# Optimization experiments

Measured on AMD Instinct MI355X. Metric: run time of the kernel, lower is better.

The kernel has to match this reference:

```python
import jax, jax.numpy as jnp
import numpy as np

N = 100000      # nodes
E = 3200000     # edges (before self-loops)
IN = 1          # input feature dim
H1, C = 4, 8    # layer1: 4 heads x 8 channels; layer2: 1 head x 8 channels
NEG_SLOPE = 0.2


def setup_inputs() -> dict:
    key = jax.random.key(0)
    ks = jax.random.split(key, 10)
    x = jax.random.normal(ks[0], (N, IN), jnp.float32)
    edge_index = jax.random.randint(ks[1], (2, E), 0, N, dtype=jnp.int32)
    # layer 1 params (GATConv(1, 8, heads=4))
    W1 = jax.random.normal(ks[2], (IN, H1 * C), jnp.float32) * 0.5
    a_src1 = jax.random.normal(ks[3], (H1, C), jnp.float32) * 0.5
    a_dst1 = jax.random.normal(ks[4], (H1, C), jnp.float32) * 0.5
    b1 = jnp.zeros((H1 * C,), jnp.float32)
    # layer 2 params (GATConv(32, 8, heads=1))
    W2 = jax.random.normal(ks[5], (H1 * C, C), jnp.float32) * 0.2
    a_src2 = jax.random.normal(ks[6], (1, C), jnp.float32) * 0.5
    a_dst2 = jax.random.normal(ks[7], (1, C), jnp.float32) * 0.5
    b2 = jnp.zeros((C,), jnp.float32)
    return {"x": x, "edge_index": edge_index, "W1": W1, "a_src1": a_src1,
            "a_dst1": a_dst1, "b1": b1, "W2": W2, "a_src2": a_src2,
            "a_dst2": a_dst2, "b2": b2}


def _gat_layer(x, src, dst, W, a_s, a_d, b, heads, ch):
    # Linear transform per head: [N, heads, ch]
    h = (x @ W).reshape(-1, heads, ch)
    # per-node attention logits
    al_s = jnp.einsum('nhc,hc->nh', h, a_s)  # [N, H]
    al_d = jnp.einsum('nhc,hc->nh', h, a_d)  # [N, H]
    # per-edge logits (message src -> dst)
    e = jax.nn.leaky_relu(al_s[src] + al_d[dst], NEG_SLOPE)  # [E', H]
    # segment softmax over incoming edges of each dst node
    m = jax.ops.segment_max(e, dst, num_segments=N)          # [N, H]
    e = jnp.exp(e - m[dst])
    s = jax.ops.segment_sum(e, dst, num_segments=N)          # [N, H]
    alpha = e / s[dst]                                       # [E', H]
    # weighted scatter-add aggregation
    out = jax.ops.segment_sum(h[src] * alpha[:, :, None], dst, num_segments=N)
    return out.reshape(N, heads * ch) + b


def reference(x, edge_index, W1, a_src1, a_dst1, b1, W2, a_src2, a_dst2, b2):
    loops = jnp.arange(N, dtype=edge_index.dtype)
    src = jnp.concatenate([edge_index[0], loops])  # add self-loops (PyG default)
    dst = jnp.concatenate([edge_index[1], loops])
    h = _gat_layer(x, src, dst, W1, a_src1, a_dst1, b1, H1, C)
    h = jax.nn.relu(h)
    out = _gat_layer(h, src, dst, W2, a_src2, a_dst2, b2, 1, C)
    return out
```

## Files before the change

kernel.cpp:

```cpp
#include <hip/hip_runtime.h>
#include <hip/hip_bf16.h>

#define NEG_SLOPE 0.2f
#define CAP 6144
#define CAPG 8192


__global__ void init_cc(int* __restrict__ gcursor,
                        const float* __restrict__ W1,
                        const float* __restrict__ as1,
                        const float* __restrict__ ad1,
                        float* __restrict__ consts) {
    int t = threadIdx.x;
    if (t < 8) {
        int h = t & 3;
        const float* a = (t < 4) ? as1 : ad1;
        float s = 0.f;
        #pragma unroll
        for (int c = 0; c < 8; ++c)
            s += W1[h * 8 + c] * a[h * 8 + c];
        consts[t] = s;
    }
    gcursor[t] = t << 13;
}

__global__ void bucket_scatter(const int* __restrict__ ei, int* __restrict__ gcursor,
                               unsigned int* __restrict__ pairs, int E) {
    __shared__ int cnt[1024];
    __shared__ int basel[1024];
    int t = threadIdx.x;
    int chunk = (E + gridDim.x - 1) / gridDim.x;
    int lo = blockIdx.x * chunk;
    int hi = min(E, lo + chunk);
    const int* dei = ei + E;
    cnt[t] = 0;
    __syncthreads();
    bool vec = ((E & 3) == 0);
    int lo4 = (lo + 3) & ~3;
    int end4 = hi & ~3;
    if (vec && end4 > lo4) {
        for (int e = lo + t; e < lo4; e += 1024)
            atomicAdd(&cnt[dei[e] >> 7], 1);
        const int4* dei4 = (const int4*)dei;
        for (int v = (lo4 >> 2) + t; v < (end4 >> 2); v += 1024) {
            int4 d = dei4[v];
            atomicAdd(&cnt[d.x >> 7], 1);
            atomicAdd(&cnt[d.y >> 7], 1);
            atomicAdd(&cnt[d.z >> 7], 1);
            atomicAdd(&cnt[d.w >> 7], 1);
        }
        for (int e = end4 + t; e < hi; e += 1024)
            atomicAdd(&cnt[dei[e] >> 7], 1);
    } else {
        for (int e = lo + t; e < hi; e += 1024)
            atomicAdd(&cnt[dei[e] >> 7], 1);
    }
    __syncthreads();
    {
        int c = cnt[t];
        basel[t] = c ? (atomicAdd(&gcursor[t], c) - (t << 13)) : 0;
        cnt[t] = 0;
    }
    __syncthreads();
    if (vec && end4 > lo4) {
        for (int e = lo + t; e < lo4; e += 1024) {
            int s = ei[e], d = dei[e];
            int bk = d >> 7;
            int off = basel[bk] + atomicAdd(&cnt[bk], 1);
            if (off < CAPG) pairs[(bk << 13) + off] = (unsigned)s | ((unsigned)(d & 127) << 17);
        }
        const int4* sei4 = (const int4*)ei;
        const int4* dei4 = (const int4*)dei;
        for (int v = (lo4 >> 2) + t; v < (end4 >> 2); v += 1024) {
            int4 sv = sei4[v];
            int4 dv = dei4[v];
            int bk0 = dv.x >> 7, bk1 = dv.y >> 7, bk2 = dv.z >> 7, bk3 = dv.w >> 7;
            int o0 = basel[bk0] + atomicAdd(&cnt[bk0], 1);
            if (o0 < CAPG) pairs[(bk0 << 13) + o0] = (unsigned)sv.x | ((unsigned)(dv.x & 127) << 17);
            int o1 = basel[bk1] + atomicAdd(&cnt[bk1], 1);
            if (o1 < CAPG) pairs[(bk1 << 13) + o1] = (unsigned)sv.y | ((unsigned)(dv.y & 127) << 17);
            int o2 = basel[bk2] + atomicAdd(&cnt[bk2], 1);
            if (o2 < CAPG) pairs[(bk2 << 13) + o2] = (unsigned)sv.z | ((unsigned)(dv.z & 127) << 17);
            int o3 = basel[bk3] + atomicAdd(&cnt[bk3], 1);
            if (o3 < CAPG) pairs[(bk3 << 13) + o3] = (unsigned)sv.w | ((unsigned)(dv.w & 127) << 17);
        }
        for (int e = end4 + t; e < hi; e += 1024) {
            int s = ei[e], d = dei[e];
            int bk = d >> 7;
            int off = basel[bk] + atomicAdd(&cnt[bk], 1);
            if (off < CAPG) pairs[(bk << 13) + off] = (unsigned)s | ((unsigned)(d & 127) << 17);
        }
    } else {
        for (int e = lo + t; e < hi; e += 1024) {
            int s = ei[e], d = dei[e];
            int bk = d >> 7;
            int off = basel[bk] + atomicAdd(&cnt[bk], 1);
            if (off < CAPG) pairs[(bk << 13) + off] = (unsigned)s | ((unsigned)(d & 127) << 17);
        }
    }
}

__global__ void l1_comb(const float* __restrict__ x,
                        const int* __restrict__ gcursor,
                        const unsigned int* __restrict__ pairs,
                        const float* __restrict__ consts,
                        const float* __restrict__ W1, const float* __restrict__ b1,
                        const float* __restrict__ W2,
                        const float* __restrict__ as2, const float* __restrict__ ad2,
                        float* __restrict__ h2, float* __restrict__ als2,
                        float* __restrict__ ald2, int N) {
    __shared__ unsigned sbuf[CAP];
    __shared__ int hcnt[128], offs[128], hcur[128];
    __shared__ float xl[128];
    int t = threadIdx.x;
    int bk = blockIdx.x;
    int node0 = bk << 7;
    int nw = min(128, N - node0);
    if (t < 128) xl[t] = (t < nw) ? x[node0 + t] : 0.f;
    float S[4], D[4];
    #pragma unroll
    for (int h = 0; h < 4; ++h) { S[h] = consts[h]; D[h] = consts[4 + h]; }
    int base = bk << 13;
    int cnt_total = min(gcursor[bk] - base, CAPG);
    int g = t >> 2, j = t & 3;
    float sacc[4] = {0.f, 0.f, 0.f, 0.f};
    float tacc[4] = {0.f, 0.f, 0.f, 0.f};
    __syncthreads();
    float xd = xl[g];
    for (int c0 = 0; c0 < cnt_total; c0 += CAP) {
        int clen = min(CAP, cnt_total - c0);
        unsigned pr[12];
        #pragma unroll
        for (int k = 0; k < 12; ++k) {
            int idx = t + (k << 9);
            pr[k] = (idx < clen) ? pairs[base + c0 + idx] : 0xFFFFFFFFu;
        }
        if (t < 128) hcnt[t] = 0;
        __syncthreads();
        #pragma unroll
        for (int k = 0; k < 12; ++k)
            if (pr[k] != 0xFFFFFFFFu) atomicAdd(&hcnt[pr[k] >> 17], 1);
        __syncthreads();
        if (t < 64) {
            int h0 = hcnt[2 * t], h1 = hcnt[2 * t + 1];
            int s = h0 + h1, sc_ = s;
            #pragma unroll
            for (int o = 1; o < 64; o <<= 1) {
                int u = __shfl_up(sc_, o);
                if (t >= o) sc_ += u;
            }
            int excl = sc_ - s;
            offs[2 * t] = excl;          hcur[2 * t] = excl;
            offs[2 * t + 1] = excl + h0; hcur[2 * t + 1] = excl + h0;
        }
        __syncthreads();
        #pragma unroll
        for (int k = 0; k < 12; ++k)
            if (pr[k] != 0xFFFFFFFFu) {
                int loc = atomicAdd(&hcur[pr[k] >> 17], 1);
                sbuf[loc] = pr[k];
            }
        __syncthreads();
        int st = offs[g], en = st + hcnt[g];
        int i = st + j;
        float xs0 = 0.f, xs1 = 0.f;
        if (i < en) xs0 = x[sbuf[i] & 131071u];
        if (i + 4 < en) xs1 = x[sbuf[i + 4] & 131071u];
        for (; i < en; i += 4) {
            float xs = xs0;
            xs0 = xs1;
            int i2 = i + 8;
            xs1 = (i2 < en) ? x[sbuf[i2] & 131071u] : 0.f;
            #pragma unroll
            for (int h = 0; h < 4; ++h) {
                float v = xs * S[h] + xd * D[h];
                v = (v > 0.f) ? v : NEG_SLOPE * v;
                float w = __expf(v);
                sacc[h] += w;
                tacc[h] = fmaf(w, xs, tacc[h]);
            }
        }
        __syncthreads();
    }
    #pragma unroll
    for (int h = 0; h < 4; ++h) {
        sacc[h] += __shfl_xor(sacc[h], 1); sacc[h] += __shfl_xor(sacc[h], 2);
        tacc[h] += __shfl_xor(tacc[h], 1); tacc[h] += __shfl_xor(tacc[h], 2);
    }
    if (j == 0 && g < nw) {
        int n = node0 + g;
        float xn = xd;
        float o[8];
        #pragma unroll
        for (int c = 0; c < 8; ++c) o[c] = 0.f;
        #pragma unroll
        for (int h = 0; h < 4; ++h) {
            float v = xn * (S[h] + D[h]);
            v = (v > 0.f) ? v : NEG_SLOPE * v;
            float ww = __expf(v);
            float s1 = ww + sacc[h];
            float t1 = ww * xn + tacc[h];
            float tt = t1 / s1;
            #pragma unroll
            for (int c = 0; c < 8; ++c) {
                float rr = fmaxf(tt * W1[h * 8 + c] + b1[h * 8 + c], 0.f);
                #pragma unroll
                for (int c2 = 0; c2 < 8; ++c2) o[c2] += rr * W2[(h * 8 + c) * 8 + c2];
            }
        }
        float as = 0.f, ad = 0.f;
        #pragma unroll
        for (int c = 0; c < 8; ++c) { as += o[c] * as2[c]; ad += o[c] * ad2[c]; }
        float4* hv = (float4*)&h2[(size_t)n * 8];
        hv[0] = make_float4(o[0], o[1], o[2], o[3]);
        hv[1] = make_float4(o[4], o[5], o[6], o[7]);
        als2[n] = as;
        ald2[n] = ad;
    }
}

__global__ void l2_comb(const int* __restrict__ gcursor,
                        const unsigned int* __restrict__ pairs,
                        const float* __restrict__ als2, const float* __restrict__ ald2,
                        const float* __restrict__ h2, const float* __restrict__ b2,
                        float* __restrict__ out, int N) {
    __shared__ unsigned sbuf[CAP];
    __shared__ int hcnt[128], offs[128], hcur[128];
    __shared__ float adl[128];
    int t = threadIdx.x;
    int bk = blockIdx.x;
    int node0 = bk << 7;
    int nw = min(128, N - node0);
    if (t < 128) adl[t] = (t < nw) ? ald2[node0 + t] : 0.f;
    int base = bk << 13;
    int cnt_total = min(gcursor[bk] - base, CAPG);
    int g = t >> 2, j = t & 3;
    float acc[9];
    #pragma unroll
    for (int c = 0; c < 9; ++c) acc[c] = 0.f;
    __syncthreads();
    float adv = adl[g];
    for (int c0 = 0; c0 < cnt_total; c0 += CAP) {
        int clen = min(CAP, cnt_total - c0);
        unsigned pr[12];
        #pragma unroll
        for (int k = 0; k < 12; ++k) {
            int idx = t + (k << 9);
            pr[k] = (idx < clen) ? pairs[base + c0 + idx] : 0xFFFFFFFFu;
        }
        if (t < 128) hcnt[t] = 0;
        __syncthreads();
        #pragma unroll
        for (int k = 0; k < 12; ++k)
            if (pr[k] != 0xFFFFFFFFu) atomicAdd(&hcnt[pr[k] >> 17], 1);
        __syncthreads();
        if (t < 64) {
            int h0 = hcnt[2 * t], h1 = hcnt[2 * t + 1];
            int s = h0 + h1, sc_ = s;
            #pragma unroll
            for (int o = 1; o < 64; o <<= 1) {
                int u = __shfl_up(sc_, o);
                if (t >= o) sc_ += u;
            }
            int excl = sc_ - s;
            offs[2 * t] = excl;          hcur[2 * t] = excl;
            offs[2 * t + 1] = excl + h0; hcur[2 * t + 1] = excl + h0;
        }
        __syncthreads();
        #pragma unroll
        for (int k = 0; k < 12; ++k)
            if (pr[k] != 0xFFFFFFFFu) {
                int loc = atomicAdd(&hcur[pr[k] >> 17], 1);
                sbuf[loc] = pr[k];
            }
        __syncthreads();
        int st = offs[g], en = st + hcnt[g];
        int i = st + j;
        float a0 = 0.f, a1 = 0.f;
        float4 hA0 = make_float4(0,0,0,0), hB0 = hA0, hA1 = hA0, hB1 = hA0;
        if (i < en) {
            int s0 = (int)(sbuf[i] & 131071u);
            a0 = als2[s0];
            const float4* q = (const float4*)&h2[(size_t)s0 * 8];
            hA0 = q[0]; hB0 = q[1];
        }
        if (i + 4 < en) {
            int s1 = (int)(sbuf[i + 4] & 131071u);
            a1 = als2[s1];
            const float4* q = (const float4*)&h2[(size_t)s1 * 8];
            hA1 = q[0]; hB1 = q[1];
        }
        for (; i < en; i += 4) {
            float a = a0; float4 hA = hA0, hB = hB0;
            a0 = a1; hA0 = hA1; hB0 = hB1;
            int i2 = i + 8;
            if (i2 < en) {
                int s2 = (int)(sbuf[i2] & 131071u);
                a1 = als2[s2];
                const float4* q = (const float4*)&h2[(size_t)s2 * 8];
                hA1 = q[0]; hB1 = q[1];
            } else {
                a1 = 0.f;
            }
            float v = a + adv;
            v = (v > 0.f) ? v : NEG_SLOPE * v;
            float w = __expf(v);
            acc[0] += w;
            acc[1] = fmaf(w, hA.x, acc[1]); acc[2] = fmaf(w, hA.y, acc[2]);
            acc[3] = fmaf(w, hA.z, acc[3]); acc[4] = fmaf(w, hA.w, acc[4]);
            acc[5] = fmaf(w, hB.x, acc[5]); acc[6] = fmaf(w, hB.y, acc[6]);
            acc[7] = fmaf(w, hB.z, acc[7]); acc[8] = fmaf(w, hB.w, acc[8]);
        }
        __syncthreads();
    }
    #pragma unroll
    for (int c = 0; c < 9; ++c) {
        acc[c] += __shfl_xor(acc[c], 1);
        acc[c] += __shfl_xor(acc[c], 2);
    }
    if (j == 0 && g < nw) {
        int n = node0 + g;
        float v = als2[n] + adv;
        v = (v > 0.f) ? v : NEG_SLOPE * v;
        float ww = __expf(v);
        const float4* hv = (const float4*)&h2[(size_t)n * 8];
        float4 ha0 = hv[0], hb0 = hv[1];
        float s2v = acc[0] + ww;
        float inv = 1.f / s2v;
        float4* ov = (float4*)&out[(size_t)n * 8];
        ov[0] = make_float4((acc[1] + ww * ha0.x) * inv + b2[0],
                            (acc[2] + ww * ha0.y) * inv + b2[1],
                            (acc[3] + ww * ha0.z) * inv + b2[2],
                            (acc[4] + ww * ha0.w) * inv + b2[3]);
        ov[1] = make_float4((acc[5] + ww * hb0.x) * inv + b2[4],
                            (acc[6] + ww * hb0.y) * inv + b2[5],
                            (acc[7] + ww * hb0.z) * inv + b2[6],
                            (acc[8] + ww * hb0.w) * inv + b2[7]);
    }
}


__global__ void prep_consts(const float* __restrict__ W1,
                            const float* __restrict__ as1,
                            const float* __restrict__ ad1,
                            float* __restrict__ consts) {
    int t = threadIdx.x;
    if (t >= 8) return;
    int h = t & 3;
    const float* a = (t < 4) ? as1 : ad1;
    float s = 0.f;
    #pragma unroll
    for (int c = 0; c < 8; ++c)
        s += W1[h * 8 + c] * a[h * 8 + c];
    consts[t] = s;
}

__global__ void edge_pass1(const int* __restrict__ ei, const float* __restrict__ x,
                           const float* __restrict__ consts,
                           float* __restrict__ s1, float* __restrict__ t1, int E, int N) {
    int e = blockIdx.x * blockDim.x + threadIdx.x;
    if (e >= E + N) return;
    int src, dst;
    if (e < E) { src = ei[e]; dst = ei[E + e]; }
    else       { src = dst = e - E; }
    float xs = x[src], xd = x[dst];
    #pragma unroll
    for (int h = 0; h < 4; ++h) {
        float v = xs * consts[h] + xd * consts[4 + h];
        v = (v > 0.f) ? v : NEG_SLOPE * v;
        float w = __expf(v);
        atomicAdd(&s1[dst * 4 + h], w);
        atomicAdd(&t1[dst * 4 + h], w * xs);
    }
}

__global__ void node_mid(const float* __restrict__ s1, const float* __restrict__ t1,
                         const float* __restrict__ W1, const float* __restrict__ b1,
                         const float* __restrict__ W2,
                         const float* __restrict__ as2, const float* __restrict__ ad2,
                         float* __restrict__ h2, float* __restrict__ als2,
                         float* __restrict__ ald2, int N) {
    int n = blockIdx.x * blockDim.x + threadIdx.x;
    if (n >= N) return;
    float o[8];
    #pragma unroll
    for (int c = 0; c < 8; ++c) o[c] = 0.f;
    #pragma unroll
    for (int h = 0; h < 4; ++h) {
        float t = t1[n * 4 + h] / s1[n * 4 + h];
        #pragma unroll
        for (int c = 0; c < 8; ++c) {
            float r = fmaxf(t * W1[h * 8 + c] + b1[h * 8 + c], 0.f);
            #pragma unroll
            for (int c2 = 0; c2 < 8; ++c2) o[c2] += r * W2[(h * 8 + c) * 8 + c2];
        }
    }
    float as = 0.f, ad = 0.f;
    #pragma unroll
    for (int c = 0; c < 8; ++c) { h2[n * 8 + c] = o[c]; as += o[c] * as2[c]; ad += o[c] * ad2[c]; }
    als2[n] = as; ald2[n] = ad;
}

__global__ void edge_pass2(const int* __restrict__ ei, const float* __restrict__ als2,
                           const float* __restrict__ ald2, const float* __restrict__ h2,
                           float* __restrict__ s2, float* __restrict__ acc2, int E, int N) {
    int e = blockIdx.x * blockDim.x + threadIdx.x;
    if (e >= E + N) return;
    int src, dst;
    if (e < E) { src = ei[e]; dst = ei[E + e]; }
    else       { src = dst = e - E; }
    float v = als2[src] + ald2[dst];
    v = (v > 0.f) ? v : NEG_SLOPE * v;
    float w = __expf(v);
    atomicAdd(&s2[dst], w);
    const float4* hs = (const float4*)&h2[src * 8];
    float4 a = hs[0], bq = hs[1];
    float* acc = &acc2[dst * 8];
    atomicAdd(&acc[0], w * a.x);  atomicAdd(&acc[1], w * a.y);
    atomicAdd(&acc[2], w * a.z);  atomicAdd(&acc[3], w * a.w);
    atomicAdd(&acc[4], w * bq.x); atomicAdd(&acc[5], w * bq.y);
    atomicAdd(&acc[6], w * bq.z); atomicAdd(&acc[7], w * bq.w);
}

__global__ void node_out(const float* __restrict__ s2, const float* __restrict__ acc2,
                         const float* __restrict__ b2, float* __restrict__ out, int N) {
    int i = blockIdx.x * blockDim.x + threadIdx.x;
    if (i >= N * 8) return;
    out[i] = acc2[i] / s2[i >> 3] + b2[i & 7];
}


extern "C" void kernel_launch(void* const* d_in, const int* in_sizes, int n_in,
                              void* d_out, int out_size, void* d_ws, size_t ws_size,
                              hipStream_t stream) {
    const float* x   = (const float*)d_in[0];
    const int*   ei  = (const int*)d_in[1];
    const float* W1  = (const float*)d_in[2];
    const float* as1 = (const float*)d_in[3];
    const float* ad1 = (const float*)d_in[4];
    const float* b1  = (const float*)d_in[5];
    const float* W2  = (const float*)d_in[6];
    const float* as2 = (const float*)d_in[7];
    const float* ad2 = (const float*)d_in[8];
    const float* b2  = (const float*)d_in[9];
    float* out = (float*)d_out;

    const int N = in_sizes[0];
    const int E = in_sizes[1] / 2;
    const int NBK = (N + 127) >> 7;

    float* ws = (float*)d_ws;
    size_t need = (size_t)(16 + 1024 + 10 * (size_t)N + (size_t)1024 * CAPG) * sizeof(float);

    if (N <= 131072 && ws_size >= need) {
        float*    consts  = ws;
        int*      gcursor = (int*)(ws + 16);
        float*    als2    = ws + 16 + 1024;
        float*    ald2    = als2 + N;
        float*    h2      = ald2 + N;
        unsigned* pairs   = (unsigned*)(h2 + 8 * (size_t)N);

        init_cc<<<1, 1024, 0, stream>>>(gcursor, W1, as1, ad1, consts);
        bucket_scatter<<<128, 1024, 0, stream>>>(ei, gcursor, pairs, E);
        l1_comb<<<NBK, 512, 0, stream>>>(x, gcursor, pairs, consts,
                                         W1, b1, W2, as2, ad2, h2, als2, ald2, N);
        l2_comb<<<NBK, 512, 0, stream>>>(gcursor, pairs, als2, ald2, h2, b2, out, N);
    } else {
        float* consts = ws;
        float* s1   = ws + 16;
        float* t1   = s1 + 4 * (size_t)N;
        float* h2   = t1 + 4 * (size_t)N;
        float* als2 = h2 + 8 * (size_t)N;
        float* ald2 = als2 + (size_t)N;
        float* s2   = ald2 + (size_t)N;
        float* acc2 = s2 + (size_t)N;

        hipMemsetAsync(ws, 0, (16 + 8 * (size_t)N) * sizeof(float), stream);
        hipMemsetAsync(s2, 0, 9 * (size_t)N * sizeof(float), stream);
        prep_consts<<<1, 64, 0, stream>>>(W1, as1, ad1, consts);
        int total = E + N;
        edge_pass1<<<(total + 255) / 256, 256, 0, stream>>>(ei, x, consts, s1, t1, E, N);
        node_mid<<<(N + 255) / 256, 256, 0, stream>>>(s1, t1, W1, b1, W2, as2, ad2, h2, als2, ald2, N);
        edge_pass2<<<(total + 255) / 256, 256, 0, stream>>>(ei, als2, ald2, h2, s2, acc2, E, N);
        node_out<<<(N * 8 + 255) / 256, 256, 0, stream>>>(s2, acc2, b2, out, N);
    }
}
```

Baseline: 198.0 us.

## Split edge bucketing into two-level radix scatter and widen combine blocks

Replaces the single-pass scatter into 1024 destination buckets with two passes: first into 64 super-buckets of 2048 nodes, then each super-bucket is split into 16 buckets of 128 nodes. The aim is more coalesced global writes and fewer scattered write streams per block. The change also doubles combine-kernel block size to 1024 threads with 8 lanes per node. It adds an extra full read and write of the edge list through an intermediate buffer, plus more workspace.

```diff
diff --git a/kernel.cpp b/kernel.cpp
--- a/kernel.cpp
+++ b/kernel.cpp
@@ -2,11 +2,12 @@
 #include <hip/hip_bf16.h>
 
 #define NEG_SLOPE 0.2f
-#define CAP 6144
-#define CAPG 8192
-
-
-__global__ void init_cc(int* __restrict__ gcursor,
+#define CAP   6144
+#define CAPG  8192
+#define CAPA  81920
+
+
+__global__ void init_cc(int* __restrict__ curA, int* __restrict__ curB,
                         const float* __restrict__ W1,
                         const float* __restrict__ as1,
                         const float* __restrict__ ad1,
@@ -21,94 +22,136 @@
             s += W1[h * 8 + c] * a[h * 8 + c];
         consts[t] = s;
     }
-    gcursor[t] = t << 13;
-}
-
-__global__ void bucket_scatter(const int* __restrict__ ei, int* __restrict__ gcursor,
-                               unsigned int* __restrict__ pairs, int E) {
-    __shared__ int cnt[1024];
-    __shared__ int basel[1024];
+    if (t < 64) curA[t] = t * CAPA;
+    curB[t] = t << 13;
+}
+
+__global__ void scatterA(const int* __restrict__ ei, int* __restrict__ curA,
+                         unsigned int* __restrict__ bufA, int E) {
+    __shared__ int cnt[64];
+    __shared__ int basel[64];
     int t = threadIdx.x;
     int chunk = (E + gridDim.x - 1) / gridDim.x;
     int lo = blockIdx.x * chunk;
     int hi = min(E, lo + chunk);
     const int* dei = ei + E;
-    cnt[t] = 0;
+    if (t < 64) cnt[t] = 0;
     __syncthreads();
     bool vec = ((E & 3) == 0);
     int lo4 = (lo + 3) & ~3;
     int end4 = hi & ~3;
     if (vec && end4 > lo4) {
         for (int e = lo + t; e < lo4; e += 1024)
-            atomicAdd(&cnt[dei[e] >> 7], 1);
+            atomicAdd(&cnt[dei[e] >> 11], 1);
         const int4* dei4 = (const int4*)dei;
         for (int v = (lo4 >> 2) + t; v < (end4 >> 2); v += 1024) {
             int4 d = dei4[v];
-            atomicAdd(&cnt[d.x >> 7], 1);
-            atomicAdd(&cnt[d.y >> 7], 1);
-            atomicAdd(&cnt[d.z >> 7], 1);
-            atomicAdd(&cnt[d.w >> 7], 1);
+            atomicAdd(&cnt[d.x >> 11], 1);
+            atomicAdd(&cnt[d.y >> 11], 1);
+            atomicAdd(&cnt[d.z >> 11], 1);
+            atomicAdd(&cnt[d.w >> 11], 1);
         }
         for (int e = end4 + t; e < hi; e += 1024)
-            atomicAdd(&cnt[dei[e] >> 7], 1);
+            atomicAdd(&cnt[dei[e] >> 11], 1);
     } else {
         for (int e = lo + t; e < hi; e += 1024)
-            atomicAdd(&cnt[dei[e] >> 7], 1);
+            atomicAdd(&cnt[dei[e] >> 11], 1);
     }
     __syncthreads();
-    {
+    if (t < 64) {
         int c = cnt[t];
-        basel[t] = c ? (atomicAdd(&gcursor[t], c) - (t << 13)) : 0;
+        basel[t] = c ? (atomicAdd(&curA[t], c) - t * CAPA) : 0;
         cnt[t] = 0;
     }
     __syncthreads();
     if (vec && end4 > lo4) {
         for (int e = lo + t; e < lo4; e += 1024) {
             int s = ei[e], d = dei[e];
-            int bk = d >> 7;
-            int off = basel[bk] + atomicAdd(&cnt[bk], 1);
-            if (off < CAPG) pairs[(bk << 13) + off] = (unsigned)s | ((unsigned)(d & 127) << 17);
+            int sp = d >> 11;
+            int off = basel[sp] + atomicAdd(&cnt[sp], 1);
+            if (off < CAPA) bufA[sp * CAPA + off] = (unsigned)s | ((unsigned)(d & 2047) << 17);
         }
         const int4* sei4 = (const int4*)ei;
         const int4* dei4 = (const int4*)dei;
         for (int v = (lo4 >> 2) + t; v < (end4 >> 2); v += 1024) {
             int4 sv = sei4[v];
             int4 dv = dei4[v];
-            int bk0 = dv.x >> 7, bk1 = dv.y >> 7, bk2 = dv.z >> 7, bk3 = dv.w >> 7;
-            int o0 = basel[bk0] + atomicAdd(&cnt[bk0], 1);
-            if (o0 < CAPG) pairs[(bk0 << 13) + o0] = (unsigned)sv.x | ((unsigned)(dv.x & 127) << 17);
-            int o1 = basel[bk1] + atomicAdd(&cnt[bk1], 1);
-            if (o1 < CAPG) pairs[(bk1 << 13) + o1] = (unsigned)sv.y | ((unsigned)(dv.y & 127) << 17);
-            int o2 = basel[bk2] + atomicAdd(&cnt[bk2], 1);
-            if (o2 < CAPG) pairs[(bk2 << 13) + o2] = (unsigned)sv.z | ((unsigned)(dv.z & 127) << 17);
-            int o3 = basel[bk3] + atomicAdd(&cnt[bk3], 1);
-            if (o3 < CAPG) pairs[(bk3 << 13) + o3] = (unsigned)sv.w | ((unsigned)(dv.w & 127) << 17);
+            int s0 = dv.x >> 11, s1 = dv.y >> 11, s2 = dv.z >> 11, s3 = dv.w >> 11;
+            int o0 = basel[s0] + atomicAdd(&cnt[s0], 1);
+            if (o0 < CAPA) bufA[s0 * CAPA + o0] = (unsigned)sv.x | ((unsigned)(dv.x & 2047) << 17);
+            int o1 = basel[s1] + atomicAdd(&cnt[s1], 1);
+            if (o1 < CAPA) bufA[s1 * CAPA + o1] = (unsigned)sv.y | ((unsigned)(dv.y & 2047) << 17);
+            int o2 = basel[s2] + atomicAdd(&cnt[s2], 1);
+            if (o2 < CAPA) bufA[s2 * CAPA + o2] = (unsigned)sv.z | ((unsigned)(dv.z & 2047) << 17);
+            int o3 = basel[s3] + atomicAdd(&cnt[s3], 1);
+            if (o3 < CAPA) bufA[s3 * CAPA + o3] = (unsigned)sv.w | ((unsigned)(dv.w & 2047) << 17);
         }
         for (int e = end4 + t; e < hi; e += 1024) {
             int s = ei[e], d = dei[e];
-            int bk = d >> 7;
-            int off = basel[bk] + atomicAdd(&cnt[bk], 1);
-            if (off < CAPG) pairs[(bk << 13) + off] = (unsigned)s | ((unsigned)(d & 127) << 17);
+            int sp = d >> 11;
+            int off = basel[sp] + atomicAdd(&cnt[sp], 1);
+            if (off < CAPA) bufA[sp * CAPA + off] = (unsigned)s | ((unsigned)(d & 2047) << 17);
         }
     } else {
         for (int e = lo + t; e < hi; e += 1024) {
             int s = ei[e], d = dei[e];
-            int bk = d >> 7;
-            int off = basel[bk] + atomicAdd(&cnt[bk], 1);
-            if (off < CAPG) pairs[(bk << 13) + off] = (unsigned)s | ((unsigned)(d & 127) << 17);
-        }
-    }
-}
-
-__global__ void l1_comb(const float* __restrict__ x,
-                        const int* __restrict__ gcursor,
-                        const unsigned int* __restrict__ pairs,
-                        const float* __restrict__ consts,
-                        const float* __restrict__ W1, const float* __restrict__ b1,
-                        const float* __restrict__ W2,
-                        const float* __restrict__ as2, const float* __restrict__ ad2,
-                        float* __restrict__ h2, float* __restrict__ als2,
-                        float* __restrict__ ald2, int N) {
+            int sp = d >> 11;
+            int off = basel[sp] + atomicAdd(&cnt[sp], 1);
+            if (off < CAPA) bufA[sp * CAPA + off] = (unsigned)s | ((unsigned)(d & 2047) << 17);
+        }
+    }
+}
+
+__global__ void scatterB(const int* __restrict__ curA, int* __restrict__ curB,
+                         const unsigned int* __restrict__ bufA,
+                         unsigned int* __restrict__ pairs) {
+    __shared__ int cnt[16];
+    __shared__ int basel[16];
+    int t = threadIdx.x;
+    int sp = blockIdx.x >> 3;
+    int part = blockIdx.x & 7;
+    int base = sp * CAPA;
+    int fill = min(curA[sp] - base, CAPA);
+    if (fill <= 0) return;
+    int lo = (fill * part) >> 3;
+    int hi = (fill * (part + 1)) >> 3;
+    for (int c0 = lo; c0 < hi; c0 += 8192) {
+        int cend = min(hi, c0 + 8192);
+        if (t < 16) cnt[t] = 0;
+        __syncthreads();
+        for (int i = c0 + t; i < cend; i += 1024)
+            atomicAdd(&cnt[(bufA[base + i] >> 24) & 15], 1);
+        __syncthreads();
+        if (t < 16) {
+            int c = cnt[t];
+            int bkg = (sp << 4) + t;
+            basel[t] = c ? (atomicAdd(&curB[bkg], c) - (bkg << 13)) : 0;
+            cnt[t] = 0;
+        }
+        __syncthreads();
+        for (int i = c0 + t; i < cend; i += 1024) {
+            unsigned p = bufA[base + i];
+            int b16 = (p >> 24) & 15;
+            int off = basel[b16] + atomicAdd(&cnt[b16], 1);
+            if (off < CAPG) {
+                int bkg = (sp << 4) + b16;
+                pairs[(bkg << 13) + off] = p & 0x00FFFFFFu;
+            }
+        }
+        __syncthreads();
+    }
+}
+
+__global__ __launch_bounds__(1024, 8)
+void l1_comb(const float* __restrict__ x,
+             const int* __restrict__ curB,
+             const unsigned int* __restrict__ pairs,
+             const float* __restrict__ consts,
+             const float* __restrict__ W1, const float* __restrict__ b1,
+             const float* __restrict__ W2,
+             const float* __restrict__ as2, const float* __restrict__ ad2,
+             float* __restrict__ h2, float* __restrict__ als2,
+             float* __restrict__ ald2, int N) {
     __shared__ unsigned sbuf[CAP];
     __shared__ int hcnt[128], offs[128], hcur[128];
     __shared__ float xl[128];
@@ -121,24 +164,24 @@
     #pragma unroll
     for (int h = 0; h < 4; ++h) { S[h] = consts[h]; D[h] = consts[4 + h]; }
     int base = bk << 13;
-    int cnt_total = min(gcursor[bk] - base, CAPG);
-    int g = t >> 2, j = t & 3;
+    int cnt_total = min(curB[bk] - base, CAPG);
+    int g = t >> 3, j = t & 7;
     float sacc[4] = {0.f, 0.f, 0.f, 0.f};
     float tacc[4] = {0.f, 0.f, 0.f, 0.f};
     __syncthreads();
     float xd = xl[g];
     for (int c0 = 0; c0 < cnt_total; c0 += CAP) {
         int clen = min(CAP, cnt_total - c0);
-        unsigned pr[12];
-        #pragma unroll
-        for (int k = 0; k < 12; ++k) {
-            int idx = t + (k << 9);
+        unsigned pr[6];
+        #pragma unroll
+        for (int k = 0; k < 6; ++k) {
+            int idx = t + (k << 10);
             pr[k] = (idx < clen) ? pairs[base + c0 + idx] : 0xFFFFFFFFu;
         }
         if (t < 128) hcnt[t] = 0;
         __syncthreads();
         #pragma unroll
-        for (int k = 0; k < 12; ++k)
+        for (int k = 0; k < 6; ++k)
             if (pr[k] != 0xFFFFFFFFu) atomicAdd(&hcnt[pr[k] >> 17], 1);
         __syncthreads();
         if (t < 64) {
@@ -155,7 +198,7 @@
         }
         __syncthreads();
         #pragma unroll
-        for (int k = 0; k < 12; ++k)
+        for (int k = 0; k < 6; ++k)
             if (pr[k] != 0xFFFFFFFFu) {
                 int loc = atomicAdd(&hcur[pr[k] >> 17], 1);
                 sbuf[loc] = pr[k];
@@ -165,11 +208,11 @@
         int i = st + j;
         float xs0 = 0.f, xs1 = 0.f;
         if (i < en) xs0 = x[sbuf[i] & 131071u];
-        if (i + 4 < en) xs1 = x[sbuf[i + 4] & 131071u];
-        for (; i < en; i += 4) {
+        if (i + 8 < en) xs1 = x[sbuf[i + 8] & 131071u];
+        for (; i < en; i += 8) {
             float xs = xs0;
             xs0 = xs1;
-            int i2 = i + 8;
+            int i2 = i + 16;
             xs1 = (i2 < en) ? x[sbuf[i2] & 131071u] : 0.f;
             #pragma unroll
             for (int h = 0; h < 4; ++h) {
@@ -185,7 +228,9 @@
     #pragma unroll
     for (int h = 0; h < 4; ++h) {
         sacc[h] += __shfl_xor(sacc[h], 1); sacc[h] += __shfl_xor(sacc[h], 2);
+        sacc[h] += __shfl_xor(sacc[h], 4);
         tacc[h] += __shfl_xor(tacc[h], 1); tacc[h] += __shfl_xor(tacc[h], 2);
+        tacc[h] += __shfl_xor(tacc[h], 4);
     }
     if (j == 0 && g < nw) {
         int n = node0 + g;
@@ -219,11 +264,12 @@
     }
 }
 
-__global__ void l2_comb(const int* __restrict__ gcursor,
-                        const unsigned int* __restrict__ pairs,
-                        const float* __restrict__ als2, const float* __restrict__ ald2,
-                        const float* __restrict__ h2, const float* __restrict__ b2,
-                        float* __restrict__ out, int N) {
+__global__ __launch_bounds__(1024, 8)
+void l2_comb(const int* __restrict__ curB,
+             const unsigned int* __restrict__ pairs,
+             const float* __restrict__ als2, const float* __restrict__ ald2,
+             const float* __restrict__ h2, const float* __restrict__ b2,
+             float* __restrict__ out, int N) {
     __shared__ unsigned sbuf[CAP];
     __shared__ int hcnt[128], offs[128], hcur[128];
     __shared__ float adl[128];
@@ -233,8 +279,8 @@
     int nw = min(128, N - node0);
     if (t < 128) adl[t] = (t < nw) ? ald2[node0 + t] : 0.f;
     int base = bk << 13;
-    int cnt_total = min(gcursor[bk] - base, CAPG);
-    int g = t >> 2, j = t & 3;
+    int cnt_total = min(curB[bk] - base, CAPG);
+    int g = t >> 3, j = t & 7;
     float acc[9];
     #pragma unroll
     for (int c = 0; c < 9; ++c) acc[c] = 0.f;
@@ -242,16 +288,16 @@
     float adv = adl[g];
     for (int c0 = 0; c0 < cnt_total; c0 += CAP) {
         int clen = min(CAP, cnt_total - c0);
-        unsigned pr[12];
-        #pragma unroll
-        for (int k = 0; k < 12; ++k) {
-            int idx = t + (k << 9);
+        unsigned pr[6];
+        #pragma unroll
+        for (int k = 0; k < 6; ++k) {
+            int idx = t + (k << 10);
             pr[k] = (idx < clen) ? pairs[base + c0 + idx] : 0xFFFFFFFFu;
         }
         if (t < 128) hcnt[t] = 0;
         __syncthreads();
         #pragma unroll
-        for (int k = 0; k < 12; ++k)
+        for (int k = 0; k < 6; ++k)
             if (pr[k] != 0xFFFFFFFFu) atomicAdd(&hcnt[pr[k] >> 17], 1);
         __syncthreads();
         if (t < 64) {
@@ -268,7 +314,7 @@
         }
         __syncthreads();
         #pragma unroll
-        for (int k = 0; k < 12; ++k)
+        for (int k = 0; k < 6; ++k)
             if (pr[k] != 0xFFFFFFFFu) {
                 int loc = atomicAdd(&hcur[pr[k] >> 17], 1);
                 sbuf[loc] = pr[k];
@@ -284,16 +330,16 @@
             const float4* q = (const float4*)&h2[(size_t)s0 * 8];
             hA0 = q[0]; hB0 = q[1];
         }
-        if (i + 4 < en) {
-            int s1 = (int)(sbuf[i + 4] & 131071u);
+        if (i + 8 < en) {
+            int s1 = (int)(sbuf[i + 8] & 131071u);
             a1 = als2[s1];
             const float4* q = (const float4*)&h2[(size_t)s1 * 8];
             hA1 = q[0]; hB1 = q[1];
         }
-        for (; i < en; i += 4) {
+        for (; i < en; i += 8) {
             float a = a0; float4 hA = hA0, hB = hB0;
             a0 = a1; hA0 = hA1; hB0 = hB1;
-            int i2 = i + 8;
+            int i2 = i + 16;
             if (i2 < en) {
                 int s2 = (int)(sbuf[i2] & 131071u);
                 a1 = als2[s2];
@@ -317,6 +363,7 @@
     for (int c = 0; c < 9; ++c) {
         acc[c] += __shfl_xor(acc[c], 1);
         acc[c] += __shfl_xor(acc[c], 2);
+        acc[c] += __shfl_xor(acc[c], 4);
     }
     if (j == 0 && g < nw) {
         int n = node0 + g;
@@ -450,21 +497,25 @@
     const int NBK = (N + 127) >> 7;
 
     float* ws = (float*)d_ws;
-    size_t need = (size_t)(16 + 1024 + 10 * (size_t)N + (size_t)1024 * CAPG) * sizeof(float);
+    size_t need = (size_t)(16 + 64 + 1024 + 10 * (size_t)N
+                           + (size_t)1024 * CAPG + (size_t)64 * CAPA) * sizeof(float);
 
     if (N <= 131072 && ws_size >= need) {
-        float*    consts  = ws;
-        int*      gcursor = (int*)(ws + 16);
-        float*    als2    = ws + 16 + 1024;
-        float*    ald2    = als2 + N;
-        float*    h2      = ald2 + N;
-        unsigned* pairs   = (unsigned*)(h2 + 8 * (size_t)N);
-
-        init_cc<<<1, 1024, 0, stream>>>(gcursor, W1, as1, ad1, consts);
-        bucket_scatter<<<128, 1024, 0, stream>>>(ei, gcursor, pairs, E);
-        l1_comb<<<NBK, 512, 0, stream>>>(x, gcursor, pairs, consts,
-                                         W1, b1, W2, as2, ad2, h2, als2, ald2, N);
-        l2_comb<<<NBK, 512, 0, stream>>>(gcursor, pairs, als2, ald2, h2, b2, out, N);
+        float*    consts = ws;
+        int*      curA   = (int*)(ws + 16);
+        int*      curB   = curA + 64;
+        float*    als2   = ws + 16 + 64 + 1024;
+        float*    ald2   = als2 + N;
+        float*    h2     = ald2 + N;
+        unsigned* pairs  = (unsigned*)(h2 + 8 * (size_t)N);
+        unsigned* bufA   = pairs + (size_t)1024 * CAPG;
+
+        init_cc<<<1, 1024, 0, stream>>>(curA, curB, W1, as1, ad1, consts);
+        scatterA<<<256, 1024, 0, stream>>>(ei, curA, bufA, E);
+        scatterB<<<512, 1024, 0, stream>>>(curA, curB, bufA, pairs);
+        l1_comb<<<NBK, 1024, 0, stream>>>(x, curB, pairs, consts,
+                                          W1, b1, W2, as2, ad2, h2, als2, ald2, N);
+        l2_comb<<<NBK, 1024, 0, stream>>>(curB, pairs, als2, ald2, h2, b2, out, N);
     } else {
         float* consts = ws;
         float* s1   = ws + 16;
```

Result: no change. 201.5 us (+1.8%).
